# Kernel tuning notes

Hardware: AMD Instinct MI355X
Metric: run time of the kernel (lower is better)

Reference implementation:

```python
import jax, jax.numpy as jnp
import numpy as np

NUM_JOINTS = 24
NUM_THETAS = NUM_JOINTS * 3  # 72
NUM_VERTS = 6890
NUM_BETAS = 10
BATCH = 512

SMPL_PARENTS = np.array([0, 0, 0, 0, 1, 2, 3, 4, 5, 6, 7, 8, 9, 9, 9,
                         12, 13, 14, 16, 17, 18, 19, 20, 21], dtype=np.int32)


def setup_inputs() -> dict:
    key = jax.random.key(0)
    ks = jax.random.split(key, 6)
    x = jax.random.normal(ks[0], (BATCH, NUM_THETAS + NUM_BETAS), dtype=jnp.float32) * 0.3
    v_template = jax.random.normal(ks[1], (NUM_VERTS, 3), dtype=jnp.float32) * 0.3
    shapedirs = jax.random.normal(ks[2], (NUM_BETAS, NUM_VERTS * 3), dtype=jnp.float32) * 0.01
    posedirs = jax.random.normal(ks[3], (207, NUM_VERTS * 3), dtype=jnp.float32) * 0.001
    Jr = jax.random.uniform(ks[4], (NUM_VERTS, NUM_JOINTS), dtype=jnp.float32)
    J_regressor = Jr / jnp.sum(Jr, axis=0, keepdims=True)
    W = jax.random.uniform(ks[5], (NUM_VERTS, NUM_JOINTS), dtype=jnp.float32)
    lbs_weights = W / jnp.sum(W, axis=1, keepdims=True)  # rows sum to 1 (skinning weights)
    parents = jnp.asarray(SMPL_PARENTS)
    return {"x": x, "v_template": v_template, "shapedirs": shapedirs,
            "J_regressor": J_regressor, "posedirs": posedirs,
            "lbs_weights": lbs_weights, "parents": parents}


def batch_rodrigues(theta):
    # theta: [N,3] axis-angle -> [N,3,3] rotation matrices
    angle = jnp.linalg.norm(theta + 1e-8, axis=1, keepdims=True)  # [N,1]
    r = theta / angle                                              # [N,3] unit axis
    cos = jnp.cos(angle)[..., None]                                # [N,1,1]
    sin = jnp.sin(angle)[..., None]
    outer = r[:, :, None] * r[:, None, :]                          # [N,3,3]
    rx, ry, rz = r[:, 0], r[:, 1], r[:, 2]
    zero = jnp.zeros_like(rx)
    K = jnp.stack([zero, -rz, ry,
                   rz, zero, -rx,
                   -ry, rx, zero], axis=1).reshape(-1, 3, 3)       # skew-symmetric
    eye = jnp.eye(3, dtype=theta.dtype)
    return cos * eye + (1.0 - cos) * outer + sin * K


def global_rigid_transformation(Rs, J, parents):
    # Rs: [B,24,3,3], J: [B,24,3] -> A: [B,24,4,4]
    B = Rs.shape[0]
    dtype = Rs.dtype
    bottom = jnp.broadcast_to(jnp.array([0, 0, 0, 1], dtype=dtype), (B, 1, 4))

    def make_A(R, t):  # R:[B,3,3], t:[B,3]
        Rt = jnp.concatenate([R, t[:, :, None]], axis=2)  # [B,3,4]
        return jnp.concatenate([Rt, bottom], axis=1)       # [B,4,4]

    parents = np.asarray(parents)
    results = [make_A(Rs[:, 0], J[:, 0])]
    for i in range(1, NUM_JOINTS):
        t_rel = J[:, i] - J[:, parents[i]]
        A_here = make_A(Rs[:, i], t_rel)
        results.append(jnp.matmul(results[parents[i]], A_here))
    results = jnp.stack(results, axis=1)  # [B,24,4,4]

    Js_w0 = jnp.concatenate([J, jnp.zeros((B, NUM_JOINTS, 1), dtype=dtype)], axis=2)  # [B,24,4]
    init_bone = jnp.einsum('bjpq,bjq->bjp', results, Js_w0)                           # [B,24,4]
    A = results - jnp.pad(init_bone[..., None], ((0, 0), (0, 0), (0, 0), (3, 0)))
    return A


def reference(x, v_template, shapedirs, J_regressor, posedirs, lbs_weights, parents):
    B = x.shape[0]
    thetas = x[:, :NUM_THETAS]
    betas = x[:, NUM_THETAS:]

    # shape blendshapes
    v_shaped = (betas @ shapedirs).reshape(B, NUM_VERTS, 3) + v_template  # [B,V,3]

    J = jnp.einsum('bvc,vj->bjc', v_shaped, J_regressor)  # [B,24,3]

    # pose rotations + pose blendshapes
    Rs = batch_rodrigues(thetas.reshape(-1, 3)).reshape(B, NUM_JOINTS, 3, 3)
    pose_feature = (Rs[:, 1:] - jnp.eye(3, dtype=x.dtype)).reshape(B, 207)
    v_posed = (pose_feature @ posedirs).reshape(B, NUM_VERTS, 3) + v_shaped

    # kinematic chain
    A = global_rigid_transformation(Rs, J, parents)  # [B,24,4,4]

    # linear blend skinning
    T = jnp.einsum('vj,bjpq->bvpq', lbs_weights, A)  # [B,V,4,4]
    v_posed_homo = jnp.concatenate(
        [v_posed, jnp.ones((B, NUM_VERTS, 1), dtype=x.dtype)], axis=2)  # [B,V,4]
    verts = jnp.einsum('bvpq,bvq->bvp', T, v_posed_homo)[:, :, :3]
    return verts
```

## Files before the change

### kernel.cpp

```cpp
#include <hip/hip_runtime.h>

#define NUM_JOINTS 24
#define NUM_VERTS  6890
#define NUM_COORDS (NUM_VERTS * 3)
#define NUM_BETAS  10
#define KTOT       217
#define KPAD       224
#define BATCH      512
#define VPAD       6912

#define WS_SJP  0
#define WS_XBF  85536
#define WS_DBF  142880
#define WS_WHBF 2465312
#define WS_AH   2575904
#define WS_AL   2706976

typedef __attribute__((ext_vector_type(8))) short short8;
typedef __attribute__((ext_vector_type(4))) float f32x4;

__device__ inline unsigned short f2bf(float f) {
    union { float f; unsigned u; } c; c.f = f;
    unsigned u = c.u;
    u += 0x7fffu + ((u >> 16) & 1u);
    return (unsigned short)(u >> 16);
}
__device__ inline float bf2f(unsigned short h) {
    union { unsigned u; float f; } c; c.u = ((unsigned)h) << 16;
    return c.f;
}

struct PBShm {
    float Rs[4][24][9];
    float Jl[4][24][3];
    float Rg[4][24][9];
    float tg[4][24][3];
    float As[4][24][12];
};

__global__ __launch_bounds__(256) void k_prep(const float* __restrict__ Jr,
                                              const float* __restrict__ sd,
                                              const float* __restrict__ pd,
                                              const float* __restrict__ vt,
                                              const float* __restrict__ w,
                                              float* __restrict__ ws) {
    __shared__ __align__(16) unsigned char smem[28928];
    const int t   = blockIdx.x;
    const int tid = threadIdx.x;
    unsigned short* whbf = (unsigned short*)(ws + WS_WHBF);
    unsigned short* dbf  = (unsigned short*)(ws + WS_DBF);

    if (t < 27) {
        const int v = t * 256 + tid;
        const bool ok = (v < NUM_VERTS);
        unsigned short row[32];
        #pragma unroll
        for (int j = 0; j < 32; ++j)
            row[j] = f2bf((ok && j < 24) ? w[v * 24 + j] : 0.f);
        #pragma unroll
        for (int i = 0; i < 4; ++i)
            *(float4*)(whbf + (size_t)v * 32 + i * 8) = *(const float4*)(&row[i * 8]);
    } else if (t < 351) {
        unsigned* L = (unsigned*)smem;
        const int c0   = (t - 27) * 64;
        const int lane = tid & 63;
        const int grp  = tid >> 6;
        const int c    = c0 + lane;
        const bool cv  = (c < NUM_COORDS);
        #pragma unroll 4
        for (int i = 0; i < 28; ++i) {
            const int p  = i * 4 + grp;
            const int k0 = 2 * p, k1 = k0 + 1;
            float v0 = 0.f, v1 = 0.f;
            if (cv) {
                v0 = (k0 < 10) ? sd[(size_t)k0 * NUM_COORDS + c]
                   : (k0 < KTOT) ? pd[(size_t)(k0 - 10) * NUM_COORDS + c] : 0.f;
                v1 = (k1 < 10) ? sd[(size_t)k1 * NUM_COORDS + c]
                   : (k1 < KTOT) ? pd[(size_t)(k1 - 10) * NUM_COORDS + c] : 0.f;
            }
            L[lane * 113 + p] = (unsigned)f2bf(v0) | ((unsigned)f2bf(v1) << 16);
        }
        __syncthreads();
        #pragma unroll
        for (int i = 0; i < 7; ++i) {
            const int idx = i * 256 + tid;
            const int row = idx / 28;
            const int q   = idx % 28;
            uint4 val;
            val.x = L[row * 113 + q * 4 + 0];
            val.y = L[row * 113 + q * 4 + 1];
            val.z = L[row * 113 + q * 4 + 2];
            val.w = L[row * 113 + q * 4 + 3];
            *(uint4*)(dbf + (size_t)(c0 + row) * KPAD + q * 8) = val;
        }
    } else {
        float* Jl = (float*)smem;
        float* S  = (float*)smem + 64 * 25;
        const int strip = t - 351;
        const int v0 = strip * 64;
        #pragma unroll
        for (int i = 0; i < 6; ++i) {
            const int idx = i * 256 + tid;
            const int v = idx / 24, j = idx % 24;
            Jl[v * 25 + j] = (v0 + v < NUM_VERTS) ? Jr[(size_t)(v0 + v) * 24 + j] : 0.f;
        }
        #pragma unroll
        for (int i = 0; i < 9; ++i) {
            const int idx = i * 256 + tid;
            if (idx < 33 * 64) {
                const int s = idx / 64, v = idx % 64;
                float val = 0.f;
                if (v0 + v < NUM_VERTS) {
                    if (s < 30) val = sd[(size_t)(s / 3) * NUM_COORDS + (size_t)(v0 + v) * 3 + (s % 3)];
                    else        val = vt[(size_t)(v0 + v) * 3 + (s - 30)];
                }
                S[s * 64 + v] = val;
            }
        }
        __syncthreads();
        float* wsp = ws + WS_SJP + (size_t)strip * 792;
        for (int o = tid; o < 792; o += 256) {
            const int s = o / 24, j = o % 24;
            float sum = 0.f;
            #pragma unroll 8
            for (int v = 0; v < 64; ++v)
                sum += S[s * 64 + v] * Jl[v * 25 + j];
            wsp[o] = sum;
        }
    }
}

__global__ __launch_bounds__(256) void k_pb(const float* __restrict__ x,
                                            const int* __restrict__ parents,
                                            float* __restrict__ ws) {
    __shared__ PBShm P;
    __shared__ float SJf[792];
    unsigned short* xbf = (unsigned short*)(ws + WS_XBF);
    unsigned short* ahi = (unsigned short*)(ws + WS_AH);
    unsigned short* alo = (unsigned short*)(ws + WS_AL);
    const int tid = threadIdx.x;

    {
        const float* wsp = ws + WS_SJP;
        for (int o = tid; o < 792; o += 256) {
            float sum = 0.f;
            for (int s2 = 0; s2 < 108; ++s2)
                sum += wsp[(size_t)s2 * 792 + o];
            SJf[o] = sum;
        }
    }
    __syncthreads();

    const int sub  = tid >> 6;
    const int lane = tid & 63;
    const int b = blockIdx.x * 4 + sub;
    const float* row = x + b * (NUM_BETAS + 72);

    if (lane < 24) {
        const int j = lane;
        const float t0 = row[3 * j + 0], t1 = row[3 * j + 1], t2 = row[3 * j + 2];
        const float a0 = t0 + 1e-8f, a1 = t1 + 1e-8f, a2 = t2 + 1e-8f;
        const float angle = sqrtf(a0 * a0 + a1 * a1 + a2 * a2);
        const float inv = 1.0f / angle;
        const float rx = t0 * inv, ry = t1 * inv, rz = t2 * inv;
        const float c = cosf(angle), sn = sinf(angle), o = 1.f - c;
        float R[9];
        R[0] = c + o * rx * rx;       R[1] = o * rx * ry - sn * rz; R[2] = o * rx * rz + sn * ry;
        R[3] = o * rx * ry + sn * rz; R[4] = c + o * ry * ry;       R[5] = o * ry * rz - sn * rx;
        R[6] = o * rx * rz - sn * ry; R[7] = o * ry * rz + sn * rx; R[8] = c + o * rz * rz;
        #pragma unroll
        for (int i = 0; i < 9; ++i) P.Rs[sub][j][i] = R[i];
        #pragma unroll
        for (int c3 = 0; c3 < 3; ++c3) {
            float s = SJf[(30 + c3) * 24 + j];
            #pragma unroll
            for (int k = 0; k < NUM_BETAS; ++k)
                s += row[72 + k] * SJf[(k * 3 + c3) * 24 + j];
            P.Jl[sub][j][c3] = s;
        }
        if (j >= 1) {
            #pragma unroll
            for (int i = 0; i < 9; ++i) {
                const float pf = R[i] - ((i == 0 || i == 4 || i == 8) ? 1.f : 0.f);
                xbf[(size_t)b * KPAD + 10 + (j - 1) * 9 + i] = f2bf(pf);
            }
        }
    }
    if (lane < NUM_BETAS) xbf[(size_t)b * KPAD + lane] = f2bf(row[72 + lane]);
    if (lane == 63) {
        #pragma unroll
        for (int k = KTOT; k < KPAD; ++k) xbf[(size_t)b * KPAD + k] = 0;
    }
    __syncthreads();

    if (lane == 0) {
        #pragma unroll
        for (int i = 0; i < 9; ++i) P.Rg[sub][0][i] = P.Rs[sub][0][i];
        #pragma unroll
        for (int c3 = 0; c3 < 3; ++c3) P.tg[sub][0][c3] = P.Jl[sub][0][c3];
        for (int i = 1; i < 24; ++i) {
            const int p = parents[i];
            float tmp[9];
            #pragma unroll
            for (int r = 0; r < 3; ++r)
                #pragma unroll
                for (int cc = 0; cc < 3; ++cc)
                    tmp[r * 3 + cc] = P.Rg[sub][p][r * 3 + 0] * P.Rs[sub][i][0 + cc] +
                                      P.Rg[sub][p][r * 3 + 1] * P.Rs[sub][i][3 + cc] +
                                      P.Rg[sub][p][r * 3 + 2] * P.Rs[sub][i][6 + cc];
            #pragma unroll
            for (int q = 0; q < 9; ++q) P.Rg[sub][i][q] = tmp[q];
            const float tr0 = P.Jl[sub][i][0] - P.Jl[sub][p][0];
            const float tr1 = P.Jl[sub][i][1] - P.Jl[sub][p][1];
            const float tr2 = P.Jl[sub][i][2] - P.Jl[sub][p][2];
            #pragma unroll
            for (int r = 0; r < 3; ++r)
                P.tg[sub][i][r] = P.Rg[sub][p][r * 3 + 0] * tr0 + P.Rg[sub][p][r * 3 + 1] * tr1 +
                                  P.Rg[sub][p][r * 3 + 2] * tr2 + P.tg[sub][p][r];
        }
    }
    __syncthreads();

    if (lane < 24) {
        const int j = lane;
        #pragma unroll
        for (int r = 0; r < 3; ++r) {
            const float tt = P.tg[sub][j][r] - (P.Rg[sub][j][r * 3 + 0] * P.Jl[sub][j][0] +
                                                P.Rg[sub][j][r * 3 + 1] * P.Jl[sub][j][1] +
                                                P.Rg[sub][j][r * 3 + 2] * P.Jl[sub][j][2]);
            P.As[sub][j][r * 4 + 0] = P.Rg[sub][j][r * 3 + 0];
            P.As[sub][j][r * 4 + 1] = P.Rg[sub][j][r * 3 + 1];
            P.As[sub][j][r * 4 + 2] = P.Rg[sub][j][r * 3 + 2];
            P.As[sub][j][r * 4 + 3] = tt;
        }
    }
    __syncthreads();

    if (lane < 32) {
        const int r = lane >> 1;
        const int half = lane & 1;
        unsigned short hi[16], lo[16];
        #pragma unroll
        for (int i = 0; i < 16; ++i) {
            const int j = half * 16 + i;
            float v = 0.f;
            if (r < 12 && j < 24) v = P.As[sub][j][r];
            const unsigned short h = f2bf(v);
            hi[i] = h;
            lo[i] = f2bf(v - bf2f(h));
        }
        unsigned short* dh = ahi + ((size_t)b * 16 + r) * 32 + half * 16;
        unsigned short* dl = alo + ((size_t)b * 16 + r) * 32 + half * 16;
        #pragma unroll
        for (int i = 0; i < 2; ++i) {
            *(float4*)(dh + i * 8) = *(const float4*)(&hi[i * 8]);
            *(float4*)(dl + i * 8) = *(const float4*)(&lo[i * 8]);
        }
    }
}

__global__ __launch_bounds__(256) void k_gemm(const float* __restrict__ vt,
                                              float* __restrict__ out,
                                              float* __restrict__ ws) {
    __shared__ __align__(16) unsigned short Xs[64 * 232];
    const unsigned short* dbf = (const unsigned short*)(ws + WS_DBF);
    const unsigned short* xbf = (const unsigned short*)(ws + WS_XBF);
    const int tid  = threadIdx.x;
    const int wave = tid >> 6;
    const int lane = tid & 63;
    const int col  = lane & 15;
    const int quad = lane >> 4;
    const int n0   = blockIdx.x * 64;
    const int nc   = n0 + wave * 16 + col;

    short8 bfrag[7];
    {
        const unsigned short* brow = dbf + (size_t)nc * KPAD + quad * 8;
        #pragma unroll
        for (int kb = 0; kb < 7; ++kb)
            bfrag[kb] = *(const short8*)(brow + kb * 32);
    }
    const float vtl = (nc < NUM_COORDS) ? vt[nc] : 0.f;
    const bool nok = (nc < NUM_COORDS);

    for (int chunk = 0; chunk < 2; ++chunk) {
        const int m0 = blockIdx.y * 128 + chunk * 64;
        __syncthreads();
        #pragma unroll
        for (int i = 0; i < 7; ++i) {
            const int c = tid + i * 256;
            const int r = c / 28;
            const int off = c % 28;
            const float4 v = *(const float4*)(xbf + (size_t)(m0 + r) * KPAD + off * 8);
            *(float4*)(&Xs[r * 232 + off * 8]) = v;
        }
        __syncthreads();

        #pragma unroll
        for (int mt = 0; mt < 4; ++mt) {
            const unsigned short* arow = &Xs[(mt * 16 + col) * 232 + quad * 8];
            f32x4 acc = {0.f, 0.f, 0.f, 0.f};
            #pragma unroll
            for (int kb = 0; kb < 7; ++kb) {
                const short8 afrag = *(const short8*)(arow + kb * 32);
                acc = __builtin_amdgcn_mfma_f32_16x16x32_bf16(afrag, bfrag[kb], acc, 0, 0, 0);
            }
            if (nok) {
                float* base = out + (size_t)(m0 + mt * 16 + quad * 4) * NUM_COORDS + nc;
                base[0]                       = acc[0] + vtl;
                base[(size_t)NUM_COORDS]      = acc[1] + vtl;
                base[(size_t)2 * NUM_COORDS]  = acc[2] + vtl;
                base[(size_t)3 * NUM_COORDS]  = acc[3] + vtl;
            }
        }
    }
}

__global__ __launch_bounds__(256) void k_skin(float* __restrict__ out,
                                              float* __restrict__ ws) {
    __shared__ float Ts[4][64 * 17];
    const unsigned short* whbf = (const unsigned short*)(ws + WS_WHBF);
    const unsigned short* ahi  = (const unsigned short*)(ws + WS_AH);
    const unsigned short* alo  = (const unsigned short*)(ws + WS_AL);
    const int tid  = threadIdx.x;
    const int wave = tid >> 6;
    const int lane = tid & 63;
    const int col  = lane & 15;
    const int quad = lane >> 4;
    const int v0   = blockIdx.x * 64;
    const int b0   = blockIdx.y * 32;

    short8 wfrag[4];
    #pragma unroll
    for (int mt = 0; mt < 4; ++mt)
        wfrag[mt] = *(const short8*)(whbf + (size_t)(v0 + mt * 16 + col) * 32 + quad * 8);

    float* ts = &Ts[wave][0];
    const int vv = v0 + lane;
    const bool vok = (vv < NUM_VERTS);

    for (int nt = wave; nt < 32; nt += 4) {
        const int b = b0 + nt;
        float* orow = out + (size_t)b * NUM_COORDS + (size_t)vv * 3;
        float h0 = 0.f, h1 = 0.f, h2 = 0.f;
        if (vok) { h0 = orow[0]; h1 = orow[1]; h2 = orow[2]; }

        const short8 bh = *(const short8*)(ahi + ((size_t)b * 16 + col) * 32 + quad * 8);
        const short8 bl = *(const short8*)(alo + ((size_t)b * 16 + col) * 32 + quad * 8);

        f32x4 acc[4];
        #pragma unroll
        for (int mt = 0; mt < 4; ++mt) {
            f32x4 z = {0.f, 0.f, 0.f, 0.f};
            z = __builtin_amdgcn_mfma_f32_16x16x32_bf16(wfrag[mt], bh, z, 0, 0, 0);
            z = __builtin_amdgcn_mfma_f32_16x16x32_bf16(wfrag[mt], bl, z, 0, 0, 0);
            acc[mt] = z;
        }
        #pragma unroll
        for (int mt = 0; mt < 4; ++mt)
            #pragma unroll
            for (int r = 0; r < 4; ++r)
                ts[(mt * 16 + quad * 4 + r) * 17 + col] = acc[mt][r];

        float Tp[12];
        #pragma unroll
        for (int i = 0; i < 12; ++i) Tp[i] = ts[lane * 17 + i];

        if (vok) {
            const float o0 = Tp[0] * h0 + Tp[1] * h1 + Tp[2]  * h2 + Tp[3];
            const float o1 = Tp[4] * h0 + Tp[5] * h1 + Tp[6]  * h2 + Tp[7];
            const float o2 = Tp[8] * h0 + Tp[9] * h1 + Tp[10] * h2 + Tp[11];
            orow[0] = o0; orow[1] = o1; orow[2] = o2;
        }
    }
}

extern "C" void kernel_launch(void* const* d_in, const int* in_sizes, int n_in,
                              void* d_out, int out_size, void* d_ws, size_t ws_size,
                              hipStream_t stream) {
    const float* x  = (const float*)d_in[0];
    const float* vt = (const float*)d_in[1];
    const float* sd = (const float*)d_in[2];
    const float* Jr = (const float*)d_in[3];
    const float* pd = (const float*)d_in[4];
    const float* w  = (const float*)d_in[5];
    const int* parents = (const int*)d_in[6];
    float* out = (float*)d_out;
    float* ws  = (float*)d_ws;

    k_prep<<<459, 256, 0, stream>>>(Jr, sd, pd, vt, w, ws);
    k_pb  <<<128, 256, 0, stream>>>(x, parents, ws);
    k_gemm<<<dim3(323, 4), 256, 0, stream>>>(vt, out, ws);
    k_skin<<<dim3(108, 16), 256, 0, stream>>>(out, ws);
}
```

Before: 163.2 us.

## Retile blendshape GEMM so each wave computes three column tiles per A fragment

The GEMM kernel now gives each wave 48 output columns (three 16-wide tiles) and each block 32 rows per chunk, with 64 rows per block instead of 128. Each A fragment read from shared memory is reused across three MFMAs, and the grid shrinks from 323x4 to 108x8 blocks. The aim is to cut LDS traffic and redundant X staging per MFMA. In exchange, each thread holds more registers for B fragments and accumulators, which may lower occupancy, and each block now computes half as many rows.

```diff
diff --git a/kernel.cpp b/kernel.cpp
--- a/kernel.cpp
+++ b/kernel.cpp
@@ -259,10 +259,10 @@
     }
 }
 
-__global__ __launch_bounds__(256) void k_gemm(const float* __restrict__ vt,
-                                              float* __restrict__ out,
-                                              float* __restrict__ ws) {
-    __shared__ __align__(16) unsigned short Xs[64 * 232];
+__global__ __launch_bounds__(256) void k_gemmA(const float* __restrict__ vt,
+                                               float* __restrict__ out,
+                                               float* __restrict__ ws) {
+    __shared__ __align__(16) unsigned short Xs[32 * 232];
     const unsigned short* dbf = (const unsigned short*)(ws + WS_DBF);
     const unsigned short* xbf = (const unsigned short*)(ws + WS_XBF);
     const int tid  = threadIdx.x;
@@ -270,47 +270,55 @@
     const int lane = tid & 63;
     const int col  = lane & 15;
     const int quad = lane >> 4;
-    const int n0   = blockIdx.x * 64;
-    const int nc   = n0 + wave * 16 + col;
-
-    short8 bfrag[7];
-    {
+    const int c0   = blockIdx.x * 192;
+
+    short8 bfrag[3][7];
+    float vtl[3];
+    #pragma unroll
+    for (int nt = 0; nt < 3; ++nt) {
+        const int nc = c0 + wave * 48 + nt * 16 + col;
         const unsigned short* brow = dbf + (size_t)nc * KPAD + quad * 8;
         #pragma unroll
         for (int kb = 0; kb < 7; ++kb)
-            bfrag[kb] = *(const short8*)(brow + kb * 32);
-    }
-    const float vtl = (nc < NUM_COORDS) ? vt[nc] : 0.f;
-    const bool nok = (nc < NUM_COORDS);
+            bfrag[nt][kb] = *(const short8*)(brow + kb * 32);
+        vtl[nt] = (nc < NUM_COORDS) ? vt[nc] : 0.f;
+    }
 
     for (int chunk = 0; chunk < 2; ++chunk) {
-        const int m0 = blockIdx.y * 128 + chunk * 64;
+        const int m0 = blockIdx.y * 64 + chunk * 32;
         __syncthreads();
         #pragma unroll
-        for (int i = 0; i < 7; ++i) {
+        for (int i = 0; i < 4; ++i) {
             const int c = tid + i * 256;
-            const int r = c / 28;
-            const int off = c % 28;
-            const float4 v = *(const float4*)(xbf + (size_t)(m0 + r) * KPAD + off * 8);
-            *(float4*)(&Xs[r * 232 + off * 8]) = v;
+            if (c < 32 * 28) {
+                const int r = c / 28, off = c % 28;
+                *(float4*)(&Xs[r * 232 + off * 8]) =
+                    *(const float4*)(xbf + (size_t)(m0 + r) * KPAD + off * 8);
+            }
         }
         __syncthreads();
 
         #pragma unroll
-        for (int mt = 0; mt < 4; ++mt) {
+        for (int mt = 0; mt < 2; ++mt) {
             const unsigned short* arow = &Xs[(mt * 16 + col) * 232 + quad * 8];
-            f32x4 acc = {0.f, 0.f, 0.f, 0.f};
+            f32x4 acc[3] = {{0.f,0.f,0.f,0.f},{0.f,0.f,0.f,0.f},{0.f,0.f,0.f,0.f}};
             #pragma unroll
             for (int kb = 0; kb < 7; ++kb) {
-                const short8 afrag = *(const short8*)(arow + kb * 32);
-                acc = __builtin_amdgcn_mfma_f32_16x16x32_bf16(afrag, bfrag[kb], acc, 0, 0, 0);
-            }
-            if (nok) {
-                float* base = out + (size_t)(m0 + mt * 16 + quad * 4) * NUM_COORDS + nc;
-                base[0]                       = acc[0] + vtl;
-                base[(size_t)NUM_COORDS]      = acc[1] + vtl;
-                base[(size_t)2 * NUM_COORDS]  = acc[2] + vtl;
-                base[(size_t)3 * NUM_COORDS]  = acc[3] + vtl;
+                const short8 af = *(const short8*)(arow + kb * 32);
+                #pragma unroll
+                for (int nt = 0; nt < 3; ++nt)
+                    acc[nt] = __builtin_amdgcn_mfma_f32_16x16x32_bf16(af, bfrag[nt][kb], acc[nt], 0, 0, 0);
+            }
+            #pragma unroll
+            for (int nt = 0; nt < 3; ++nt) {
+                const int nc = c0 + wave * 48 + nt * 16 + col;
+                if (nc < NUM_COORDS) {
+                    float* base = out + (size_t)(m0 + mt * 16 + quad * 4) * NUM_COORDS + nc;
+                    base[0]                      = acc[nt][0] + vtl[nt];
+                    base[(size_t)NUM_COORDS]     = acc[nt][1] + vtl[nt];
+                    base[(size_t)2 * NUM_COORDS] = acc[nt][2] + vtl[nt];
+                    base[(size_t)3 * NUM_COORDS] = acc[nt][3] + vtl[nt];
+                }
             }
         }
     }
@@ -388,8 +396,8 @@
     float* out = (float*)d_out;
     float* ws  = (float*)d_ws;
 
-    k_prep<<<459, 256, 0, stream>>>(Jr, sd, pd, vt, w, ws);
-    k_pb  <<<128, 256, 0, stream>>>(x, parents, ws);
-    k_gemm<<<dim3(323, 4), 256, 0, stream>>>(vt, out, ws);
-    k_skin<<<dim3(108, 16), 256, 0, stream>>>(out, ws);
-}
+    k_prep <<<459, 256, 0, stream>>>(Jr, sd, pd, vt, w, ws);
+    k_pb   <<<128, 256, 0, stream>>>(x, parents, ws);
+    k_gemmA<<<dim3(108, 8), 256, 0, stream>>>(vt, out, ws);
+    k_skin <<<dim3(108, 16), 256, 0, stream>>>(out, ws);
+}
```

Result: no change. 161.1 us (-1.3%).
